# Optimization experiments

Hardware: AMD Instinct MI355X
Metric: run time of the kernel (lower is better)

Reference implementation:

```python
import jax, jax.numpy as jnp
import numpy as np

N, F_IN, F_OUT = 8192, 256, 256
NEG_BIG = jnp.float32(-9e15)


def setup_inputs() -> dict:
    key = jax.random.key(0)
    k1, k2, k3, k4 = jax.random.split(key, 4)
    h = jax.random.normal(k1, (N, F_IN), dtype=jnp.float32)
    adj = jax.random.randint(k2, (N, N), 0, 2, dtype=jnp.int32)
    # nn.Linear(in, out): weight [out, in], bias [out]
    lim = 1.0 / np.sqrt(F_IN)
    W = jax.random.uniform(k3, (F_OUT, F_IN), dtype=jnp.float32, minval=-lim, maxval=lim)
    b = jax.random.uniform(k4, (F_OUT,), dtype=jnp.float32, minval=-lim, maxval=lim)
    return {"h": h, "adj": adj, "W": W, "b": b}


def reference(h, adj, W, b):
    n = h.shape[0]
    scale = 1.0 / jnp.sqrt(jnp.asarray(h.shape[1], h.dtype))
    # attention = h @ h.T / sqrt(d)   -> [N, N]
    att = jnp.matmul(h, h.T) * scale
    # masked softmax over rows
    A = jax.nn.softmax(jnp.where(adj > 0, att, NEG_BIG), axis=1)
    eye = jnp.eye(n, dtype=A.dtype)
    A = (A + eye) * 0.5
    # first `k` rows overwritten with identity, k = count of nonzeros in adj[:, 0]
    k = jnp.sum(adj[:, 0] != 0)
    row_is_identity = jnp.arange(n)[:, None] < k  # [N, 1] broadcast mask
    A = jnp.where(row_is_identity, eye, A)
    h_new = jnp.matmul(h, W.T) + b
    return jax.nn.relu(jnp.matmul(A, h_new))
```

## Files before the change

### kernel.cpp

```cpp
#include <hip/hip_runtime.h>


typedef __attribute__((ext_vector_type(8))) short short8;
typedef __attribute__((ext_vector_type(4))) float f32x4;

#define NN 8192
#define DD 256
#define NEGB -1.2983e16f

__device__ __forceinline__ unsigned short f2bf(float f) {
  unsigned u = __builtin_bit_cast(unsigned, f);
  u += 0x7FFFu + ((u >> 16) & 1u);
  return (unsigned short)(u >> 16);
}
__device__ __forceinline__ float bf2f(unsigned short s) {
  unsigned u = ((unsigned)s) << 16;
  return __builtin_bit_cast(float, u);
}
__device__ __forceinline__ f32x4 mfma16(short8 a, short8 b, f32x4 c) {
  return __builtin_amdgcn_mfma_f32_16x16x32_bf16(a, b, c, 0, 0, 0);
}
__device__ __forceinline__ void gld16(const unsigned short* g, unsigned short* l) {
  __builtin_amdgcn_global_load_lds(
      (const __attribute__((address_space(1))) void*)g,
      (__attribute__((address_space(3))) void*)l, 16, 0, 0);
}

__global__ __launch_bounds__(256) void prep_k(const float* __restrict__ h,
                                              const float* __restrict__ W,
                                              const int* __restrict__ adj,
                                              unsigned short* __restrict__ hQf,
                                              unsigned short* __restrict__ Wf,
                                              int* __restrict__ kout) {
  const int bx = blockIdx.x, tid = threadIdx.x;
  if (bx < 2048) {
    int gid = bx * 256 + tid;
    int i = gid >> 6, k4 = (gid & 63) * 4;
    float4 v = *(const float4*)(h + (size_t)i * DD + k4);
    size_t off = ((size_t)((i >> 4) * 8 + (k4 >> 5)) * 64 +
                  (((k4 >> 3) & 3) * 16 + (i & 15))) * 8 + (k4 & 7);
    ushort4 o;
    o.x = f2bf(v.x); o.y = f2bf(v.y); o.z = f2bf(v.z); o.w = f2bf(v.w);
    *(ushort4*)(hQf + off) = o;
  } else if (bx < 2080) {
    __shared__ int red[256];
    int gid = (bx - 2048) * 256 + tid;
    red[tid] = (adj[(size_t)gid * NN] != 0);
    __syncthreads();
    for (int off = 128; off; off >>= 1) {
      if (tid < off) red[tid] += red[tid + off];
      __syncthreads();
    }
    if (tid == 0) atomicAdd(kout, red[0]);
  } else {
    int gid = (bx - 2080) * 256 + tid;
    int l = gid & 63, f = gid >> 6, n16 = f >> 3, kk = f & 7;
    int lr = l & 15, lg = l >> 4;
    const float* src = W + (size_t)(n16 * 16 + lr) * DD + kk * 32 + lg * 8;
    float4 w0 = *(const float4*)src, w1 = *(const float4*)(src + 4);
    short8 o;
    o[0] = (short)f2bf(w0.x); o[1] = (short)f2bf(w0.y);
    o[2] = (short)f2bf(w0.z); o[3] = (short)f2bf(w0.w);
    o[4] = (short)f2bf(w1.x); o[5] = (short)f2bf(w1.y);
    o[6] = (short)f2bf(w1.z); o[7] = (short)f2bf(w1.w);
    *(short8*)(Wf + (size_t)gid * 8) = o;
  }
}

__global__ __launch_bounds__(256) void hnew_k(const unsigned short* __restrict__ hQf,
                                              const unsigned short* __restrict__ Wf,
                                              const float* __restrict__ bias,
                                              unsigned short* __restrict__ hnb,
                                              unsigned short* __restrict__ hnV) {
  const int tid = threadIdx.x, w = tid >> 6, l = tid & 63, lr = l & 15, lg = l >> 4;
  const int row0 = (blockIdx.x >> 1) * 64 + w * 16;
  const int nt0 = (blockIdx.x & 1) * 8;

  short8 a[8];
#pragma unroll
  for (int kk = 0; kk < 8; ++kk)
    a[kk] = *(const short8*)(hQf + ((size_t)((row0 >> 4) * 8 + kk) * 64 + l) * 8);

  f32x4 acc[8];
#pragma unroll
  for (int nt = 0; nt < 8; ++nt) acc[nt] = (f32x4){0.f, 0.f, 0.f, 0.f};

#pragma unroll
  for (int kk = 0; kk < 8; ++kk)
#pragma unroll
    for (int nt = 0; nt < 8; ++nt) {
      short8 bf = *(const short8*)(Wf + ((size_t)((nt0 + nt) * 8 + kk) * 64 + l) * 8);
      acc[nt] = mfma16(a[kk], bf, acc[nt]);
    }
  const int rowbase = row0 + lg * 4;
#pragma unroll
  for (int nt = 0; nt < 8; ++nt) {
    const int col = (nt0 + nt) * 16 + lr;
    const float bv = bias[col];
    unsigned short r16[4];
#pragma unroll
    for (int q = 0; q < 4; ++q) r16[q] = f2bf(acc[nt][q] + bv);
#pragma unroll
    for (int q = 0; q < 4; ++q) hnb[(size_t)(rowbase + q) * DD + col] = r16[q];
    ushort4 o4 = {r16[0], r16[1], r16[2], r16[3]};
    *(ushort4*)(hnV + ((size_t)((rowbase >> 5) * 16 + nt0 + nt) * 64 +
                       ((rowbase >> 3) & 3) * 16 + lr) * 8 + (rowbase & 7)) = o4;
  }
}

__global__ __launch_bounds__(256, 2) void attn_k(
    const unsigned short* __restrict__ hQf, const unsigned short* __restrict__ hnV,
    const int* __restrict__ adj, const int* __restrict__ kptr,
    float* __restrict__ pl, unsigned short* __restrict__ pO, int T) {
  __shared__ __align__(16) unsigned short sK[2][8192];
  __shared__ __align__(16) unsigned short sV[2][8192];
  __shared__ __align__(16) unsigned short sP[4][16][40];

  const int tid = threadIdx.x, w = tid >> 6, l = tid & 63, lr = l & 15, lg = l >> 4;
  const int c = blockIdx.x, ty = blockIdx.y;
  const int i0 = ty * 64;
  const int kid = *kptr;
  if (i0 + 64 <= kid) return;

  const int r0 = i0 + w * 16;

  short8 qf[8];
#pragma unroll
  for (int kk = 0; kk < 8; ++kk)
    qf[kk] = *(const short8*)(hQf + ((size_t)((r0 >> 4) * 8 + kk) * 64 + l) * 8);

  f32x4 Oacc[16];
#pragma unroll
  for (int nt = 0; nt < 16; ++nt) Oacc[nt] = (f32x4){0.f, 0.f, 0.f, 0.f};
  float lsum[4] = {0.f, 0.f, 0.f, 0.f};
  const float c1 = 0.09016844005556021f;

  int arow[4];
#pragma unroll
  for (int q = 0; q < 4; ++q) arow[q] = (r0 + lg * 4 + q) * NN;

  const int jt0 = c * T;

  {
    const unsigned short* srcK = hQf + (size_t)jt0 * 8192;
    const unsigned short* srcV = hnV + (size_t)jt0 * 8192;
#pragma unroll
    for (int s = 0; s < 4; ++s) {
      const int so = (w * 4 + s) * 512;
      gld16(srcK + so + l * 8, &sK[0][so]);
      gld16(srcV + so + l * 8, &sV[0][so]);
    }
  }
  int avA[8], avB[8];
#pragma unroll
  for (int nt = 0; nt < 2; ++nt)
#pragma unroll
    for (int q = 0; q < 4; ++q)
      avA[nt * 4 + q] = adj[(size_t)arow[q] + jt0 * 32 + nt * 16 + lr];
  __syncthreads();

#define ATTN_ITER(T_IDX, CUR, MC, MN)                                          \
  {                                                                            \
    const int t_ = (T_IDX);                                                    \
    if (t_ + 1 < T) {    \
      const int jn = jt0 + t_ + 1;                                             \
      const unsigned short* srcK = hQf + (size_t)jn * 8192;                    \
      const unsigned short* srcV = hnV + (size_t)jn * 8192;                    \
      _Pragma("unroll") for (int s = 0; s < 4; ++s) {                          \
        const int so = (w * 4 + s) * 512;                                      \
        gld16(srcK + so + l * 8, &sK[(CUR) ^ 1][so]);                          \
        gld16(srcV + so + l * 8, &sV[(CUR) ^ 1][so]);                          \
      }                                                                        \
      _Pragma("unroll") for (int nt = 0; nt < 2; ++nt)                         \
        _Pragma("unroll") for (int q = 0; q < 4; ++q)                          \
          MN[nt * 4 + q] = adj[(size_t)arow[q] + jn * 32 + nt * 16 + lr];      \
    }                                                                          \
    f32x4 S2[2];                                                               \
    S2[0] = (f32x4){0.f, 0.f, 0.f, 0.f};                                       \
    S2[1] = (f32x4){0.f, 0.f, 0.f, 0.f};                                       \
    __builtin_amdgcn_s_setprio(1);                                             \
    _Pragma("unroll") for (int kk = 0; kk < 8; ++kk)                           \
      _Pragma("unroll") for (int nt = 0; nt < 2; ++nt) {                       \
        short8 bf = *(const short8*)(&sK[(CUR)][(nt * 8 + kk) * 512 + l * 8]); \
        S2[nt] = mfma16(qf[kk], bf, S2[nt]);                                   \
      }                                                                        \
    __builtin_amdgcn_s_setprio(0);                                             \
    float p0[4], p1[4];                                                        \
    _Pragma("unroll") for (int q = 0; q < 4; ++q) {                            \
      float sv0 = MC[q] ? fminf(S2[0][q] * c1, 60.f) : NEGB;                   \
      float sv1 = MC[4 + q] ? fminf(S2[1][q] * c1, 60.f) : NEGB;               \
      p0[q] = __builtin_amdgcn_exp2f(sv0);                                     \
      p1[q] = __builtin_amdgcn_exp2f(sv1);                                     \
      lsum[q] += p0[q] + p1[q];                                                \
    }                                                                          \
    _Pragma("unroll") for (int q = 0; q < 4; ++q) {                            \
      sP[w][lg * 4 + q][lr] = f2bf(p0[q]);                                     \
      sP[w][lg * 4 + q][16 + lr] = f2bf(p1[q]);                                \
    }                                                                          \
    short8 pa = *(const short8*)(&sP[w][lr][lg * 8]);                          \
    __builtin_amdgcn_s_setprio(1);                                             \
    _Pragma("unroll") for (int cnt = 0; cnt < 16; ++cnt) {                     \
      short8 vf = *(const short8*)(&sV[(CUR)][cnt * 512 + l * 8]);             \
      Oacc[cnt] = mfma16(pa, vf, Oacc[cnt]);                                   \
    }                                                                          \
    __builtin_amdgcn_s_setprio(0);                                             \
    __syncthreads();                                                           \
  }

  for (int tt = 0; tt < T; tt += 2) {
    ATTN_ITER(tt, 0, avA, avB);
    ATTN_ITER(tt + 1, 1, avB, avA);
  }
#undef ATTN_ITER

#pragma unroll
  for (int q = 0; q < 4; ++q) {
#pragma unroll
    for (int off = 1; off < 16; off <<= 1) lsum[q] += __shfl_xor(lsum[q], off);
    if (lr == 0) pl[(size_t)c * NN + r0 + lg * 4 + q] = lsum[q];
  }
#pragma unroll
  for (int cnt = 0; cnt < 16; ++cnt)
#pragma unroll
    for (int q = 0; q < 4; ++q) {
      int row = r0 + lg * 4 + q;
      pO[((size_t)c * NN + row) * DD + cnt * 16 + lr] = f2bf(Oacc[cnt][q]);
    }
}

__global__ __launch_bounds__(256) void comb_k(const float* __restrict__ pl,
                                              const unsigned short* __restrict__ pO,
                                              const unsigned short* __restrict__ hnb,
                                              const int* __restrict__ kptr,
                                              float* __restrict__ out, int S) {
  const int row = blockIdx.x * 4 + (threadIdx.x >> 6);
  const int col = (threadIdx.x & 63) * 4;
  const int kid = *kptr;
  ushort4 hv = *(const ushort4*)(hnb + (size_t)row * DD + col);
  float v0 = bf2f(hv.x), v1 = bf2f(hv.y), v2 = bf2f(hv.z), v3 = bf2f(hv.w);
  float4 r;
  if (row < kid) {
    r.x = v0; r.y = v1; r.z = v2; r.w = v3;
  } else {
    float L = 0.f, a0 = 0.f, a1 = 0.f, a2 = 0.f, a3 = 0.f;
    for (int cc = 0; cc < S; ++cc) {
      L += pl[(size_t)cc * NN + row];
      ushort4 ov = *(const ushort4*)(pO + ((size_t)cc * NN + row) * DD + col);
      a0 += bf2f(ov.x); a1 += bf2f(ov.y); a2 += bf2f(ov.z); a3 += bf2f(ov.w);
    }
    float inv = 0.5f / L;
    r.x = a0 * inv + 0.5f * v0; r.y = a1 * inv + 0.5f * v1;
    r.z = a2 * inv + 0.5f * v2; r.w = a3 * inv + 0.5f * v3;
  }
  r.x = fmaxf(r.x, 0.f); r.y = fmaxf(r.y, 0.f);
  r.z = fmaxf(r.z, 0.f); r.w = fmaxf(r.w, 0.f);
  *(float4*)(out + (size_t)row * DD + col) = r;
}

extern "C" void kernel_launch(void* const* d_in, const int* in_sizes, int n_in,
                              void* d_out, int out_size, void* d_ws, size_t ws_size,
                              hipStream_t stream) {
  const float* h = (const float*)d_in[0];
  const int* adj = (const int*)d_in[1];
  const float* W = (const float*)d_in[2];
  const float* b = (const float*)d_in[3];
  float* out = (float*)d_out;

  char* ws = (char*)d_ws;
  const size_t MB4 = (size_t)NN * DD * 2;
  int* kbuf = (int*)ws;
  unsigned short* hQf = (unsigned short*)(ws + 256);
  unsigned short* hnb = (unsigned short*)(ws + 256 + MB4);
  unsigned short* hnV = (unsigned short*)(ws + 256 + 2 * MB4);
  unsigned short* Wf = (unsigned short*)(ws + 256 + 3 * MB4);
  char* dyn = ws + 256 + 3 * MB4 + (256 << 10);

  size_t fixed = 256 + 3 * MB4 + (256 << 10);
  int S = 16;
  while (S > 1 && fixed + (size_t)S * NN * (DD * 2 + 4) > ws_size) S >>= 1;
  const int T = 256 / S;

  float* pl = (float*)dyn;
  unsigned short* pO = (unsigned short*)(pl + (size_t)S * NN);

  hipMemsetAsync(kbuf, 0, 4, stream);
  hipLaunchKernelGGL(prep_k, dim3(2112), dim3(256), 0, stream, h, W, adj, hQf, Wf, kbuf);
  hipLaunchKernelGGL(hnew_k, dim3(256), dim3(256), 0, stream, hQf, Wf, b, hnb, hnV);
  hipLaunchKernelGGL(attn_k, dim3(S, NN / 64), dim3(256), 0, stream,
                     hQf, hnV, adj, kbuf, pl, pO, T);
  hipLaunchKernelGGL(comb_k, dim3(NN / 4), dim3(256), 0, stream, pl, pO, hnb, kbuf, out, S);
}
```

Baseline: 106.1 us.

## Fuse h bf16 conversion into hnew, keep P in registers via transposed QK

```diff
diff --git a/kernel.cpp b/kernel.cpp
--- a/kernel.cpp
+++ b/kernel.cpp
@@ -26,25 +26,14 @@
       (__attribute__((address_space(3))) void*)l, 16, 0, 0);
 }
 
-__global__ __launch_bounds__(256) void prep_k(const float* __restrict__ h,
-                                              const float* __restrict__ W,
+__global__ __launch_bounds__(256) void prep_k(const float* __restrict__ W,
                                               const int* __restrict__ adj,
-                                              unsigned short* __restrict__ hQf,
                                               unsigned short* __restrict__ Wf,
                                               int* __restrict__ kout) {
   const int bx = blockIdx.x, tid = threadIdx.x;
-  if (bx < 2048) {
+  if (bx < 32) {
+    __shared__ int red[256];
     int gid = bx * 256 + tid;
-    int i = gid >> 6, k4 = (gid & 63) * 4;
-    float4 v = *(const float4*)(h + (size_t)i * DD + k4);
-    size_t off = ((size_t)((i >> 4) * 8 + (k4 >> 5)) * 64 +
-                  (((k4 >> 3) & 3) * 16 + (i & 15))) * 8 + (k4 & 7);
-    ushort4 o;
-    o.x = f2bf(v.x); o.y = f2bf(v.y); o.z = f2bf(v.z); o.w = f2bf(v.w);
-    *(ushort4*)(hQf + off) = o;
-  } else if (bx < 2080) {
-    __shared__ int red[256];
-    int gid = (bx - 2048) * 256 + tid;
     red[tid] = (adj[(size_t)gid * NN] != 0);
     __syncthreads();
     for (int off = 128; off; off >>= 1) {
@@ -53,7 +42,7 @@
     }
     if (tid == 0) atomicAdd(kout, red[0]);
   } else {
-    int gid = (bx - 2080) * 256 + tid;
+    int gid = (bx - 32) * 256 + tid;
     int l = gid & 63, f = gid >> 6, n16 = f >> 3, kk = f & 7;
     int lr = l & 15, lg = l >> 4;
     const float* src = W + (size_t)(n16 * 16 + lr) * DD + kk * 32 + lg * 8;
@@ -67,35 +56,45 @@
   }
 }
 
-__global__ __launch_bounds__(256) void hnew_k(const unsigned short* __restrict__ hQf,
+__global__ __launch_bounds__(256) void hnew_k(const float* __restrict__ h,
                                               const unsigned short* __restrict__ Wf,
                                               const float* __restrict__ bias,
+                                              unsigned short* __restrict__ hQf,
                                               unsigned short* __restrict__ hnb,
                                               unsigned short* __restrict__ hnV) {
   const int tid = threadIdx.x, w = tid >> 6, l = tid & 63, lr = l & 15, lg = l >> 4;
-  const int row0 = (blockIdx.x >> 1) * 64 + w * 16;
-  const int nt0 = (blockIdx.x & 1) * 8;
+  const int row0 = blockIdx.x * 64 + w * 16;
+  const int j16 = row0 >> 4;
 
   short8 a[8];
 #pragma unroll
+  for (int kk = 0; kk < 8; ++kk) {
+    const float* src = h + (size_t)(row0 + lr) * DD + kk * 32 + lg * 8;
+    float4 v0 = *(const float4*)src, v1 = *(const float4*)(src + 4);
+    short8 o;
+    o[0] = (short)f2bf(v0.x); o[1] = (short)f2bf(v0.y);
+    o[2] = (short)f2bf(v0.z); o[3] = (short)f2bf(v0.w);
+    o[4] = (short)f2bf(v1.x); o[5] = (short)f2bf(v1.y);
+    o[6] = (short)f2bf(v1.z); o[7] = (short)f2bf(v1.w);
+    a[kk] = o;
+    *(short8*)(hQf + ((size_t)(j16 * 8 + kk) * 64 + l) * 8) = o;
+  }
+
+  f32x4 acc[16];
+#pragma unroll
+  for (int nt = 0; nt < 16; ++nt) acc[nt] = (f32x4){0.f, 0.f, 0.f, 0.f};
+#pragma unroll
   for (int kk = 0; kk < 8; ++kk)
-    a[kk] = *(const short8*)(hQf + ((size_t)((row0 >> 4) * 8 + kk) * 64 + l) * 8);
-
-  f32x4 acc[8];
-#pragma unroll
-  for (int nt = 0; nt < 8; ++nt) acc[nt] = (f32x4){0.f, 0.f, 0.f, 0.f};
-
-#pragma unroll
-  for (int kk = 0; kk < 8; ++kk)
-#pragma unroll
-    for (int nt = 0; nt < 8; ++nt) {
-      short8 bf = *(const short8*)(Wf + ((size_t)((nt0 + nt) * 8 + kk) * 64 + l) * 8);
+#pragma unroll
+    for (int nt = 0; nt < 16; ++nt) {
+      short8 bf = *(const short8*)(Wf + ((size_t)(nt * 8 + kk) * 64 + l) * 8);
       acc[nt] = mfma16(a[kk], bf, acc[nt]);
     }
   const int rowbase = row0 + lg * 4;
-#pragma unroll
-  for (int nt = 0; nt < 8; ++nt) {
-    const int col = (nt0 + nt) * 16 + lr;
+  const int eb = ((rowbase >> 4) & 1) * 4;
+#pragma unroll
+  for (int nt = 0; nt < 16; ++nt) {
+    const int col = nt * 16 + lr;
     const float bv = bias[col];
     unsigned short r16[4];
 #pragma unroll
@@ -103,8 +102,8 @@
 #pragma unroll
     for (int q = 0; q < 4; ++q) hnb[(size_t)(rowbase + q) * DD + col] = r16[q];
     ushort4 o4 = {r16[0], r16[1], r16[2], r16[3]};
-    *(ushort4*)(hnV + ((size_t)((rowbase >> 5) * 16 + nt0 + nt) * 64 +
-                       ((rowbase >> 3) & 3) * 16 + lr) * 8 + (rowbase & 7)) = o4;
+    *(ushort4*)(hnV + (((size_t)(rowbase >> 5) * 16 + nt) * 64 + lg * 16 + lr) * 8 +
+                eb) = o4;
   }
 }
 
@@ -114,7 +113,6 @@
     float* __restrict__ pl, unsigned short* __restrict__ pO, int T) {
   __shared__ __align__(16) unsigned short sK[2][8192];
   __shared__ __align__(16) unsigned short sV[2][8192];
-  __shared__ __align__(16) unsigned short sP[4][16][40];
 
   const int tid = threadIdx.x, w = tid >> 6, l = tid & 63, lr = l & 15, lg = l >> 4;
   const int c = blockIdx.x, ty = blockIdx.y;
@@ -132,12 +130,10 @@
   f32x4 Oacc[16];
 #pragma unroll
   for (int nt = 0; nt < 16; ++nt) Oacc[nt] = (f32x4){0.f, 0.f, 0.f, 0.f};
-  float lsum[4] = {0.f, 0.f, 0.f, 0.f};
+  float lsum = 0.f;
   const float c1 = 0.09016844005556021f;
 
-  int arow[4];
-#pragma unroll
-  for (int q = 0; q < 4; ++q) arow[q] = (r0 + lg * 4 + q) * NN;
+  const size_t arow = (size_t)(r0 + lr) * NN;
 
   const int jt0 = c * T;
 
@@ -152,17 +148,18 @@
     }
   }
   int avA[8], avB[8];
-#pragma unroll
-  for (int nt = 0; nt < 2; ++nt)
-#pragma unroll
-    for (int q = 0; q < 4; ++q)
-      avA[nt * 4 + q] = adj[(size_t)arow[q] + jt0 * 32 + nt * 16 + lr];
+  {
+    int4 t0 = *(const int4*)(adj + arow + jt0 * 32 + lg * 4);
+    int4 t1 = *(const int4*)(adj + arow + jt0 * 32 + 16 + lg * 4);
+    avA[0] = t0.x; avA[1] = t0.y; avA[2] = t0.z; avA[3] = t0.w;
+    avA[4] = t1.x; avA[5] = t1.y; avA[6] = t1.z; avA[7] = t1.w;
+  }
   __syncthreads();
 
 #define ATTN_ITER(T_IDX, CUR, MC, MN)                                          \
   {                                                                            \
     const int t_ = (T_IDX);                                                    \
-    if (t_ + 1 < T) {    \
+    if (t_ + 1 < T) {                        \
       const int jn = jt0 + t_ + 1;                                             \
       const unsigned short* srcK = hQf + (size_t)jn * 8192;                    \
       const unsigned short* srcV = hnV + (size_t)jn * 8192;                    \
@@ -171,9 +168,10 @@
         gld16(srcK + so + l * 8, &sK[(CUR) ^ 1][so]);                          \
         gld16(srcV + so + l * 8, &sV[(CUR) ^ 1][so]);                          \
       }                                                                        \
-      _Pragma("unroll") for (int nt = 0; nt < 2; ++nt)                         \
-        _Pragma("unroll") for (int q = 0; q < 4; ++q)                          \
-          MN[nt * 4 + q] = adj[(size_t)arow[q] + jn * 32 + nt * 16 + lr];      \
+      int4 t0 = *(const int4*)(adj + arow + jn * 32 + lg * 4);                 \
+      int4 t1 = *(const int4*)(adj + arow + jn * 32 + 16 + lg * 4);            \
+      MN[0] = t0.x; MN[1] = t0.y; MN[2] = t0.z; MN[3] = t0.w;                  \
+      MN[4] = t1.x; MN[5] = t1.y; MN[6] = t1.z; MN[7] = t1.w;                  \
     }                                                                          \
     f32x4 S2[2];                                                               \
     S2[0] = (f32x4){0.f, 0.f, 0.f, 0.f};                                       \
@@ -181,23 +179,23 @@
     __builtin_amdgcn_s_setprio(1);                                             \
     _Pragma("unroll") for (int kk = 0; kk < 8; ++kk)                           \
       _Pragma("unroll") for (int nt = 0; nt < 2; ++nt) {                       \
-        short8 bf = *(const short8*)(&sK[(CUR)][(nt * 8 + kk) * 512 + l * 8]); \
-        S2[nt] = mfma16(qf[kk], bf, S2[nt]);                                   \
+        short8 kf = *(const short8*)(&sK[(CUR)][(nt * 8 + kk) * 512 + l * 8]); \
+        S2[nt] = mfma16(kf, qf[kk], S2[nt]);                 \
       }                                                                        \
     __builtin_amdgcn_s_setprio(0);                                             \
-    float p0[4], p1[4];                                                        \
-    _Pragma("unroll") for (int q = 0; q < 4; ++q) {                            \
-      float sv0 = MC[q] ? fminf(S2[0][q] * c1, 60.f) : NEGB;                   \
-      float sv1 = MC[4 + q] ? fminf(S2[1][q] * c1, 60.f) : NEGB;               \
-      p0[q] = __builtin_amdgcn_exp2f(sv0);                                     \
-      p1[q] = __builtin_amdgcn_exp2f(sv1);                                     \
-      lsum[q] += p0[q] + p1[q];                                                \
+    float p[2][4];                                                             \
+    _Pragma("unroll") for (int nt = 0; nt < 2; ++nt)                           \
+      _Pragma("unroll") for (int q = 0; q < 4; ++q) {                          \
+        float sv = MC[nt * 4 + q] ? fminf(S2[nt][q] * c1, 60.f) : NEGB;        \
+        p[nt][q] = __builtin_amdgcn_exp2f(sv);                                 \
+      }                                                                        \
+    lsum += ((p[0][0] + p[0][1]) + (p[0][2] + p[0][3])) +                      \
+            ((p[1][0] + p[1][1]) + (p[1][2] + p[1][3]));                       \
+    short8 pa;                                                                 \
+    _Pragma("unroll") for (int e = 0; e < 4; ++e) {                            \
+      pa[e] = (short)f2bf(p[0][e]);                                            \
+      pa[e + 4] = (short)f2bf(p[1][e]);                                        \
     }                                                                          \
-    _Pragma("unroll") for (int q = 0; q < 4; ++q) {                            \
-      sP[w][lg * 4 + q][lr] = f2bf(p0[q]);                                     \
-      sP[w][lg * 4 + q][16 + lr] = f2bf(p1[q]);                                \
-    }                                                                          \
-    short8 pa = *(const short8*)(&sP[w][lr][lg * 8]);                          \
     __builtin_amdgcn_s_setprio(1);                                             \
     _Pragma("unroll") for (int cnt = 0; cnt < 16; ++cnt) {                     \
       short8 vf = *(const short8*)(&sV[(CUR)][cnt * 512 + l * 8]);             \
@@ -213,12 +211,9 @@
   }
 #undef ATTN_ITER
 
-#pragma unroll
-  for (int q = 0; q < 4; ++q) {
-#pragma unroll
-    for (int off = 1; off < 16; off <<= 1) lsum[q] += __shfl_xor(lsum[q], off);
-    if (lr == 0) pl[(size_t)c * NN + r0 + lg * 4 + q] = lsum[q];
-  }
+  lsum += __shfl_xor(lsum, 16);
+  lsum += __shfl_xor(lsum, 32);
+  if (lg == 0) pl[(size_t)c * NN + r0 + lr] = lsum;
 #pragma unroll
   for (int cnt = 0; cnt < 16; ++cnt)
 #pragma unroll
@@ -284,8 +279,9 @@
   unsigned short* pO = (unsigned short*)(pl + (size_t)S * NN);
 
   hipMemsetAsync(kbuf, 0, 4, stream);
-  hipLaunchKernelGGL(prep_k, dim3(2112), dim3(256), 0, stream, h, W, adj, hQf, Wf, kbuf);
-  hipLaunchKernelGGL(hnew_k, dim3(256), dim3(256), 0, stream, hQf, Wf, b, hnb, hnV);
+  hipLaunchKernelGGL(prep_k, dim3(64), dim3(256), 0, stream, W, adj, Wf, kbuf);
+  hipLaunchKernelGGL(hnew_k, dim3(NN / 64), dim3(256), 0, stream,
+                     h, Wf, b, hQf, hnb, hnV);
   hipLaunchKernelGGL(attn_k, dim3(S, NN / 64), dim3(256), 0, stream,
                      hQf, hnV, adj, kbuf, pl, pO, T);
   hipLaunchKernelGGL(comb_k, dim3(NN / 4), dim3(256), 0, stream, pl, pO, hnb, kbuf, out, S);
```

Result: no change. 107.2 us (+1.1%).
